# Kernel optimization log

Hardware: AMD Instinct MI355X
Metric: run time of the kernel (lower is better)

## Reference

```python
import jax, jax.numpy as jnp
import numpy as np

ALPHA = 0.2          # LeakyReLU negative slope (Alpha)
NEG_INF = -9e15      # mask value used by pygat-style GAT


def _masked_attention(Wh, a_src, a_dst, mask):
    """Wh: [H,N,d], a_src/a_dst: [H,d], mask: [N,N] (nonzero = edge).
    Returns attention-aggregated features [H,N,d]."""
    f_src = jnp.einsum('hnd,hd->hn', Wh, a_src)   # [H,N]
    f_dst = jnp.einsum('hnd,hd->hn', Wh, a_dst)   # [H,N]
    e = jax.nn.leaky_relu(f_src[:, :, None] + f_dst[:, None, :], ALPHA)  # [H,N,N]
    e = jnp.where(mask[None, :, :] > 0, e, NEG_INF)
    att = jax.nn.softmax(e, axis=-1)              # masked softmax over neighbors
    return jnp.einsum('hnm,hmd->hnd', att, Wh)    # [H,N,d]


def setup_inputs() -> dict:
    key = jax.random.key(0)
    ks = jax.random.split(key, 8)
    N, F_in, D, H = 4096, 512, 64, 8
    x = jax.random.normal(ks[0], (N, F_in), dtype=jnp.float32)
    adj = jax.random.randint(ks[1], (N, N), 0, 2, dtype=jnp.int32)
    s = 0.1
    W = jax.random.normal(ks[2], (H, F_in, D), dtype=jnp.float32) * s
    a_src = jax.random.normal(ks[3], (H, D), dtype=jnp.float32) * s
    a_dst = jax.random.normal(ks[4], (H, D), dtype=jnp.float32) * s
    W_o = jax.random.normal(ks[5], (H * D, D), dtype=jnp.float32) * s
    ao_src = jax.random.normal(ks[6], (D,), dtype=jnp.float32) * s
    ao_dst = jax.random.normal(ks[7], (D,), dtype=jnp.float32) * s
    return {"x": x, "adj": adj, "W": W, "a_src": a_src, "a_dst": a_dst,
            "W_o": W_o, "ao_src": ao_src, "ao_dst": ao_dst}


def reference(x, adj, W, a_src, a_dst, W_o, ao_src, ao_dst):
    N = x.shape[0]
    # --- multi-head layer (concat=True: ELU per head, concat on feature dim) ---
    Wh = jnp.einsum('nf,hfd->hnd', x, W)                     # [H,N,d]
    h1 = jax.nn.elu(_masked_attention(Wh, a_src, a_dst, adj))  # [H,N,d]
    h_cat = jnp.transpose(h1, (1, 0, 2)).reshape(N, -1)      # [N, H*d]
    # --- output head (concat=False: no ELU inside layer) ---
    Who = (h_cat @ W_o)[None]                                # [1,N,d]
    h2 = _masked_attention(Who, ao_src[None], ao_dst[None], adj)[0]  # [N,d]
    # GAT.forward: activation (ELU) then log_softmax over dim=1
    return jax.nn.log_softmax(jax.nn.elu(h2), axis=1)
```

## Files before the change

kernel.cpp:

```cpp
#include <hip/hip_runtime.h>
#include <hip/hip_bf16.h>
#include <math.h>

#define N_NODES 4096
#define FDIM 512
#define D 64
#define H 8
#define NWORDS (N_NODES / 64)
#define S1 4
#define S2 16

typedef __attribute__((ext_vector_type(8))) short bf16x8;
typedef __attribute__((ext_vector_type(4))) float f32x4;
typedef __attribute__((ext_vector_type(8))) _Float16 f16x8;
typedef __attribute__((ext_vector_type(2))) _Float16 f16x2;
typedef __attribute__((ext_vector_type(4))) unsigned int u32x4;

__device__ inline short f2h(float x) {
    _Float16 h = (_Float16)x;
    return __builtin_bit_cast(short, h);
}
__device__ inline float h2f(unsigned short u) {
    return (float)__builtin_bit_cast(_Float16, u);
}
__device__ inline f16x2 bcH(unsigned int u) { return __builtin_bit_cast(f16x2, u); }

__device__ inline int sext_bit(unsigned int v, int j) {
#if defined(__has_builtin) && __has_builtin(__builtin_amdgcn_sbfe)
    return __builtin_amdgcn_sbfe((int)v, j, 1);
#else
    return ((int)(v << (31 - j))) >> 31;
#endif
}

__device__ inline unsigned fenc(float f) {
    unsigned u = __builtin_bit_cast(unsigned, f);
    return (u & 0x80000000u) ? ~u : (u | 0x80000000u);
}
__device__ inline float fdec(unsigned e) {
    unsigned u = (e & 0x80000000u) ? (e & 0x7FFFFFFFu) : ~e;
    return __builtin_bit_cast(float, u);
}

__device__ inline void gl2lds16(const void* g, void* l) {
#if defined(__has_builtin) && __has_builtin(__builtin_amdgcn_global_load_lds)
    __builtin_amdgcn_global_load_lds(
        (const __attribute__((address_space(1))) unsigned int*)g,
        (__attribute__((address_space(3))) unsigned int*)l, 16, 0, 0);
#else
    *(uint4*)l = *(const uint4*)g;
#endif
}

#define NB_BITS (N_NODES * N_NODES / 2048)
#define NB_X    (N_NODES * FDIM / 1024)
#define NB_W    (H * FDIM * D / 256)
#define NB_WO   (FDIM * D / 256)
__global__ void k_pre(const int* __restrict__ adj, const float* __restrict__ x,
                      const float* __restrict__ W, const float* __restrict__ Wo,
                      unsigned int* __restrict__ bits32, short* __restrict__ Xbf,
                      short* __restrict__ WF, short* __restrict__ WoF,
                      float* __restrict__ cm1, float* __restrict__ cm2,
                      unsigned* __restrict__ gmaxe1, unsigned* __restrict__ gmaxe2) {
    const int b = blockIdx.x, t = threadIdx.x;
    if (b == 0) {
        for (int i = t; i < H * D; i += 256) cm1[i] = 0.f;
        if (t < D) cm2[t] = 0.f;
        if (t < H) gmaxe1[t] = 0u;
        if (t == 0) gmaxe2[0] = 0u;
        return;
    }
    if (b < 1 + NB_BITS) {
        const int tid  = (b - 1) * 256 + t;
        const size_t e0 = (size_t)tid * 8;
        int4 a0 = *(const int4*)&adj[e0];
        int4 a1 = *(const int4*)&adj[e0 + 4];
        unsigned by = (unsigned)(a0.x != 0)       | ((unsigned)(a0.y != 0) << 1)
                    | ((unsigned)(a0.z != 0) << 2) | ((unsigned)(a0.w != 0) << 3)
                    | ((unsigned)(a1.x != 0) << 4) | ((unsigned)(a1.y != 0) << 5)
                    | ((unsigned)(a1.z != 0) << 6) | ((unsigned)(a1.w != 0) << 7);
        unsigned v = by | (__shfl_xor((int)by, 1) << 8);
        v = v | ((unsigned)__shfl_xor((int)v, 2) << 16);
        if ((t & 3) == 0) bits32[tid >> 2] = v;
        return;
    }
    if (b < 1 + NB_BITS + NB_X) {
        const size_t i4 = ((size_t)(b - 1 - NB_BITS) * 256 + t) * 4;
        float4 v = *(const float4*)&x[i4];
        ushort4 o;
        o.x = (unsigned short)f2h(v.x); o.y = (unsigned short)f2h(v.y);
        o.z = (unsigned short)f2h(v.z); o.w = (unsigned short)f2h(v.w);
        *(ushort4*)&Xbf[i4] = o;
        return;
    }
    if (b < 1 + NB_BITS + NB_X + NB_W) {
        const size_t idx = (size_t)(b - 1 - NB_BITS - NB_X) * 256 + t;
        const int d = idx & 63;
        const int k = (int)(idx >> 6) & 511;
        const int h = (int)(idx >> 15);
        WF[(((size_t)h * 64 + (k >> 3)) * 64 + d) * 8 + (k & 7)] = f2h(W[idx]);
        return;
    }
    {
        const size_t idx = (size_t)(b - 1 - NB_BITS - NB_X - NB_W) * 256 + t;
        const int d = idx & 63;
        const int k = (int)(idx >> 6);
        WoF[(((size_t)(k >> 3)) * 64 + d) * 8 + (k & 7)] = f2h(Wo[idx]);
    }
}

__global__ void __launch_bounds__(256) k_gemm(
    const short* __restrict__ Xbf, const short* __restrict__ WF,
    const float* __restrict__ av, const float* __restrict__ bv,
    short* __restrict__ WBout, float* __restrict__ fs, float* __restrict__ fd,
    unsigned* __restrict__ gmaxe, float* __restrict__ cm) {
    const int h  = blockIdx.y;
    const int i0 = blockIdx.x * 64;
    const int t = threadIdx.x, w = t >> 6, lane = t & 63;
    const int li = lane & 15, quad = lane >> 4, k0 = quad * 8;
    const int row_a = i0 + w * 16 + li;
    const short* __restrict__ Xr  = Xbf + (size_t)row_a * FDIM;
    const short* __restrict__ WFh = WF + (size_t)h * 64 * D * 8;

    f32x4 c0 = {0.f, 0.f, 0.f, 0.f}, c1 = c0, c2 = c0, c3 = c0;
    #pragma unroll 4
    for (int kt = 0; kt < FDIM; kt += 32) {
        f16x8 a = __builtin_bit_cast(f16x8, *(const bf16x8*)&Xr[kt + k0]);
        const short* bb = WFh + (size_t)((kt >> 3) + quad) * (D * 8) + li * 8;
        f16x8 b0 = __builtin_bit_cast(f16x8, *(const bf16x8*)(bb));
        f16x8 b1 = __builtin_bit_cast(f16x8, *(const bf16x8*)(bb + 128));
        f16x8 b2 = __builtin_bit_cast(f16x8, *(const bf16x8*)(bb + 256));
        f16x8 b3 = __builtin_bit_cast(f16x8, *(const bf16x8*)(bb + 384));
        c0 = __builtin_amdgcn_mfma_f32_16x16x32_f16(a, b0, c0, 0, 0, 0);
        c1 = __builtin_amdgcn_mfma_f32_16x16x32_f16(a, b1, c1, 0, 0, 0);
        c2 = __builtin_amdgcn_mfma_f32_16x16x32_f16(a, b2, c2, 0, 0, 0);
        c3 = __builtin_amdgcn_mfma_f32_16x16x32_f16(a, b3, c3, 0, 0, 0);
    }
    float av4[4], bv4[4];
    #pragma unroll
    for (int t4 = 0; t4 < 4; ++t4) {
        av4[t4] = av[h * D + t4 * 16 + li];
        bv4[t4] = bv[h * D + t4 * 16 + li];
    }
    float tiles[4][4];
    #pragma unroll
    for (int r = 0; r < 4; ++r) { tiles[0][r] = c0[r]; tiles[1][r] = c1[r]; tiles[2][r] = c2[r]; tiles[3][r] = c3[r]; }

    __shared__ float csum[4][64];
    __shared__ float red[4];
    float fdmax = -INFINITY;
    float s4[4] = {0.f, 0.f, 0.f, 0.f};

    #pragma unroll
    for (int r = 0; r < 4; ++r) {
        const int row = i0 + w * 16 + quad * 4 + r;
        float pa = 0.f, pb = 0.f;
        #pragma unroll
        for (int t4 = 0; t4 < 4; ++t4) {
            const float v = tiles[t4][r];
            const int d = t4 * 16 + li;
            WBout[((size_t)h * (N_NODES / 8) + (row >> 3)) * (D * 8) + d * 8 + (row & 7)] = f2h(v);
            pa += v * av4[t4];
            pb += v * bv4[t4];
            s4[t4] += v;
        }
        #pragma unroll
        for (int off = 1; off < 16; off <<= 1) {
            pa += __shfl_xor(pa, off);
            pb += __shfl_xor(pb, off);
        }
        if (li == 0) {
            fs[(size_t)h * N_NODES + row] = pa;
            fd[(size_t)h * N_NODES + row] = pb;
        }
        fdmax = fmaxf(fdmax, pb);
    }
    fdmax = fmaxf(fdmax, __shfl_xor(fdmax, 16));
    fdmax = fmaxf(fdmax, __shfl_xor(fdmax, 32));
    if (lane == 0) red[w] = fdmax;
    #pragma unroll
    for (int t4 = 0; t4 < 4; ++t4) {
        s4[t4] += __shfl_xor(s4[t4], 16);
        s4[t4] += __shfl_xor(s4[t4], 32);
    }
    if (quad == 0)
        #pragma unroll
        for (int t4 = 0; t4 < 4; ++t4) csum[w][t4 * 16 + li] = s4[t4];
    __syncthreads();
    if (t == 0)
        atomicMax(gmaxe + h, fenc(fmaxf(fmaxf(red[0], red[1]), fmaxf(red[2], red[3]))));
    if (t < 64)
        atomicAdd(&cm[h * D + t],
                  (csum[0][t] + csum[1][t] + csum[2][t] + csum[3][t]) * (1.f / (float)N_NODES));
}

__global__ void __launch_bounds__(128, 2) k_accum(
    const unsigned int* __restrict__ bits32,
    const short* __restrict__ WB,
    const float* __restrict__ fsb, const float* __restrict__ fdb,
    const unsigned* __restrict__ gmaxe,
    short* __restrict__ num, float* __restrict__ den, int kslab) {

    __shared__ __align__(16) short Bt[2][16 * 64 * 8];
    __shared__ __align__(16) short Esh[1024];
    __shared__ __align__(16) short Gsh[1024];

    const int h = blockIdx.y, i0 = blockIdx.x * 128, slab = blockIdx.z;
    const int t = threadIdx.x, w = t >> 6, lane = t & 63;
    const int li = lane & 15, quad = lane >> 4, k0 = quad * 8;
    const size_t ho = (size_t)h * N_NODES;
    const float  gm = fdec(gmaxe[h]);
    const float* __restrict__ fd = fdb + ho;
    const short* __restrict__ Bh = WB + (size_t)h * (N_NODES / 8) * D * 8;

    const int k_beg = slab * kslab;
    const int ntile = kslab / 128;

    auto stage = [&](int buf, int jtile) {
        const short* src = Bh + (size_t)(jtile >> 3) * (D * 8);
        #pragma unroll
        for (int p = 0; p < 8; ++p)
            gl2lds16(src + (size_t)(p * 128 + t) * 8, &Bt[buf][(p * 128 + t) * 8]);
    };

    int bito[4];
    #pragma unroll
    for (int f = 0; f < 4; ++f)
        bito[f] = (i0 + w * 64 + f * 16 + li) * (NWORDS * 2);
    uint4 bw[4];
    #pragma unroll
    for (int f = 0; f < 4; ++f)
        bw[f] = *(const uint4*)&bits32[(size_t)bito[f] + (k_beg >> 5)];
    stage(0, k_beg);
    for (int jj = t * 2; jj < kslab; jj += 256) {
        float2 f2 = *(const float2*)&fd[k_beg + jj];
        f16x2 ep = {(_Float16)__expf(f2.x - gm), (_Float16)__expf(f2.y - gm)};
        f16x2 gp = {(_Float16)__expf(0.2f * (f2.x - gm)),
                    (_Float16)__expf(0.2f * (f2.y - gm))};
        *(f16x2*)&Esh[jj] = ep;
        *(f16x2*)&Gsh[jj] = gp;
    }
    f16x2 Rp[4];
    #pragma unroll
    for (int f = 0; f < 4; ++f) {
        const float rv = __expf(-0.8f * (fsb[ho + i0 + w * 64 + f * 16 + li] + gm));
        const _Float16 rh = (_Float16)rv;
        Rp[f] = (f16x2){rh, rh};
    }

    f32x4 acc[4][4], c5[4];
    #pragma unroll
    for (int f = 0; f < 4; ++f) {
        #pragma unroll
        for (int q = 0; q < 4; ++q) acc[f][q] = (f32x4){0.f, 0.f, 0.f, 0.f};
        c5[f] = (f32x4){0.f, 0.f, 0.f, 0.f};
    }
    bf16x8 ones_;
    #pragma unroll
    for (int j = 0; j < 8; ++j) ones_[j] = (short)0x3C00;
    const f16x8 ones = __builtin_bit_cast(f16x8, ones_);

    __syncthreads();

    for (int tile = 0; tile < ntile; ++tile) {
        const int jt = k_beg + tile * 128;
        __builtin_amdgcn_s_barrier();
        if (tile > 0) {
            #pragma unroll
            for (int f = 0; f < 4; ++f)
                bw[f] = *(const uint4*)&bits32[(size_t)bito[f] + (jt >> 5)];
        }
        if (tile + 1 < ntile) {
            stage((tile + 1) & 1, jt + 128);
            asm volatile("s_waitcnt vmcnt(8)" ::: "memory");
        } else {
            asm volatile("s_waitcnt vmcnt(0)" ::: "memory");
        }
        __builtin_amdgcn_s_barrier();

        const short* Bl = Bt[tile & 1];
        const short* Ee = Esh + tile * 128;
        const short* Gg = Gsh + tile * 128;
        #pragma unroll
        for (int s = 0; s < 4; ++s) {
            const uint4 Eu = *(const uint4*)&Ee[s * 32 + k0];
            const uint4 Gu = *(const uint4*)&Gg[s * 32 + k0];
            f16x2 Ep[4] = {bcH(Eu.x), bcH(Eu.y), bcH(Eu.z), bcH(Eu.w)};
            f16x2 Gp[4] = {bcH(Gu.x), bcH(Gu.y), bcH(Gu.z), bcH(Gu.w)};
            const short* bb = Bl + (size_t)((s * 4 + quad) * 64 + li) * 8;
            f16x8 b0 = __builtin_bit_cast(f16x8, *(const bf16x8*)(bb));
            f16x8 b1 = __builtin_bit_cast(f16x8, *(const bf16x8*)(bb + 128));
            f16x8 b2 = __builtin_bit_cast(f16x8, *(const bf16x8*)(bb + 256));
            f16x8 b3 = __builtin_bit_cast(f16x8, *(const bf16x8*)(bb + 384));
            #pragma unroll
            for (int f = 0; f < 4; ++f) {
                const unsigned int wsel = (s == 0) ? bw[f].x : (s == 1) ? bw[f].y
                                        : (s == 2) ? bw[f].z : bw[f].w;
                const unsigned int byt = (wsel >> k0) & 0xFFu;
                u32x4 au;
                #pragma unroll
                for (int d2 = 0; d2 < 4; ++d2) {
                    const unsigned mw = (unsigned)__builtin_amdgcn_perm(
                        (unsigned)sext_bit(byt, 2 * d2 + 1),
                        (unsigned)sext_bit(byt, 2 * d2), 0x05040100u);
                    const f16x2 tv = Gp[d2] * Rp[f];
                    const f16x2 pv = __builtin_elementwise_max(Ep[d2], tv);
                    au[d2] = __builtin_bit_cast(unsigned, pv) & mw;
                }
                const f16x8 a = __builtin_bit_cast(f16x8, au);
                __builtin_amdgcn_s_setprio(1);
                acc[f][0] = __builtin_amdgcn_mfma_f32_16x16x32_f16(a, b0, acc[f][0], 0, 0, 0);
                acc[f][1] = __builtin_amdgcn_mfma_f32_16x16x32_f16(a, b1, acc[f][1], 0, 0, 0);
                acc[f][2] = __builtin_amdgcn_mfma_f32_16x16x32_f16(a, b2, acc[f][2], 0, 0, 0);
                acc[f][3] = __builtin_amdgcn_mfma_f32_16x16x32_f16(a, b3, acc[f][3], 0, 0, 0);
                c5[f]     = __builtin_amdgcn_mfma_f32_16x16x32_f16(a, ones, c5[f], 0, 0, 0);
                __builtin_amdgcn_s_setprio(0);
            }
        }
    }

    const size_t so = (size_t)(slab * gridDim.y + h);
    #pragma unroll
    for (int f = 0; f < 4; ++f) {
        #pragma unroll
        for (int t4 = 0; t4 < 4; ++t4)
            #pragma unroll
            for (int r = 0; r < 4; ++r) {
                const int row = i0 + w * 64 + f * 16 + quad * 4 + r;
                num[(so * N_NODES + row) * D + t4 * 16 + li] = f2h(acc[f][t4][r]);
            }
        if (li == 0)
            #pragma unroll
            for (int r = 0; r < 4; ++r)
                den[so * N_NODES + i0 + w * 64 + f * 16 + quad * 4 + r] = c5[f][r];
    }
}

__global__ void k_post1(const short* __restrict__ num, const float* __restrict__ den,
                        const float* __restrict__ colmean, short* __restrict__ hcat) {
    const int h   = blockIdx.y;
    const int i0  = blockIdx.x * 64;
    const int t   = threadIdx.x;
    const int row = i0 + (t >> 2);
    const int cb  = (t & 3) * 16;
    const size_t HN = (size_t)gridDim.y * N_NODES;
    const size_t r0 = (size_t)h * N_NODES + row;
    float dsum = 0.f;
    #pragma unroll
    for (int s = 0; s < S1; ++s) dsum += den[s * HN + r0];
    const bool  uni  = !(dsum > 0.f);
    const float linv = uni ? 0.f : 1.f / dsum;
    #pragma unroll
    for (int c = 0; c < 4; ++c) {
        const int col = cb + c * 4;
        float4 v = {0.f, 0.f, 0.f, 0.f};
        #pragma unroll
        for (int s = 0; s < S1; ++s) {
            ushort4 a = *(const ushort4*)&num[(s * HN + r0) * D + col];
            v.x += h2f(a.x); v.y += h2f(a.y); v.z += h2f(a.z); v.w += h2f(a.w);
        }
        v.x *= linv; v.y *= linv; v.z *= linv; v.w *= linv;
        if (uni) v = *(const float4*)&colmean[h * D + col];
        v.x = v.x > 0.f ? v.x : __expf(v.x) - 1.f;
        v.y = v.y > 0.f ? v.y : __expf(v.y) - 1.f;
        v.z = v.z > 0.f ? v.z : __expf(v.z) - 1.f;
        v.w = v.w > 0.f ? v.w : __expf(v.w) - 1.f;
        ushort4 o;
        o.x = (unsigned short)f2h(v.x); o.y = (unsigned short)f2h(v.y);
        o.z = (unsigned short)f2h(v.z); o.w = (unsigned short)f2h(v.w);
        *(ushort4*)&hcat[(size_t)row * (H * D) + h * D + col] = o;
    }
}

__global__ void k_lsm(const short* __restrict__ num, const float* __restrict__ den,
                      const float* __restrict__ cm, float* __restrict__ out) {
    const int n    = blockIdx.x * 4 + (threadIdx.x >> 6);
    const int lane = threadIdx.x & 63;
    float v = 0.f, ds = 0.f;
    #pragma unroll
    for (int s = 0; s < S2; ++s)
        v += h2f((unsigned short)num[((size_t)s * N_NODES + n) * D + lane]);
    #pragma unroll
    for (int s = 0; s < S2; ++s) ds += den[(size_t)s * N_NODES + n];
    v = (ds > 0.f) ? v / ds : cm[lane];
    v = v > 0.f ? v : __expf(v) - 1.f;
    float mx = v;
    #pragma unroll
    for (int off = 32; off > 0; off >>= 1) mx = fmaxf(mx, __shfl_xor(mx, off));
    float ex = __expf(v - mx);
    float sum = ex;
    #pragma unroll
    for (int off = 32; off > 0; off >>= 1) sum += __shfl_xor(sum, off);
    out[(size_t)n * D + lane] = (v - mx) - __logf(sum);
}

extern "C" void kernel_launch(void* const* d_in, const int* in_sizes, int n_in,
                              void* d_out, int out_size, void* d_ws, size_t ws_size,
                              hipStream_t stream) {
    const float* x      = (const float*)d_in[0];
    const int*   adj    = (const int*)d_in[1];
    const float* W      = (const float*)d_in[2];
    const float* a_src  = (const float*)d_in[3];
    const float* a_dst  = (const float*)d_in[4];
    const float* W_o    = (const float*)d_in[5];
    const float* ao_src = (const float*)d_in[6];
    const float* ao_dst = (const float*)d_in[7];
    float* out = (float*)d_out;

    char* wsp = (char*)d_ws;
    size_t off = 0;
    auto alloc = [&](size_t bytes) -> void* {
        void* p = wsp + off;
        off += (bytes + 255) & ~(size_t)255;
        return p;
    };
    unsigned* adj_bits = (unsigned*)alloc((size_t)N_NODES * NWORDS * 8);
    short*    Xbf   = (short*)alloc((size_t)N_NODES * FDIM * 2);
    short*    WF1   = (short*)alloc((size_t)H * 64 * D * 8 * 2);
    short*    WoF   = (short*)alloc((size_t)64 * D * 8 * 2);
    short*    WhB   = (short*)alloc((size_t)H * N_NODES * D * 2);
    float*    fs1   = (float*)alloc((size_t)H * N_NODES * 4);
    float*    fd1   = (float*)alloc((size_t)H * N_NODES * 4);
    unsigned* gme1  = (unsigned*)alloc((size_t)H * 4);
    float*    cm1   = (float*)alloc((size_t)H * D * 4);
    short*    num1  = (short*)alloc((size_t)S1 * H * N_NODES * D * 2);
    float*    den1  = (float*)alloc((size_t)S1 * H * N_NODES * 4);
    short*    hcat  = (short*)alloc((size_t)N_NODES * H * D * 2);
    short*    WhoB  = (short*)alloc((size_t)N_NODES * D * 2);
    float*    fs2   = (float*)alloc((size_t)N_NODES * 4);
    float*    fd2   = (float*)alloc((size_t)N_NODES * 4);
    unsigned* gme2  = (unsigned*)alloc(4);
    float*    cm2   = (float*)alloc((size_t)D * 4);
    short*    num2  = (short*)alloc((size_t)S2 * N_NODES * D * 2);
    float*    den2  = (float*)alloc((size_t)S2 * N_NODES * 4);

    k_pre  <<<dim3(1 + NB_BITS + NB_X + NB_W + NB_WO), dim3(256), 0, stream>>>(
        adj, x, W, W_o, adj_bits, Xbf, WF1, WoF, cm1, cm2, gme1, gme2);

    k_gemm <<<dim3(N_NODES / 64, H), dim3(256), 0, stream>>>(Xbf, WF1, a_src, a_dst,
                                                             WhB, fs1, fd1, gme1, cm1);
    k_accum<<<dim3(N_NODES / 128, H, S1), dim3(128), 0, stream>>>(adj_bits, WhB, fs1, fd1, gme1,
                                                                  num1, den1, N_NODES / S1);
    k_post1<<<dim3(N_NODES / 64, H), dim3(256), 0, stream>>>(num1, den1, cm1, hcat);

    k_gemm <<<dim3(N_NODES / 64, 1), dim3(256), 0, stream>>>(hcat, WoF, ao_src, ao_dst,
                                                             WhoB, fs2, fd2, gme2, cm2);
    k_accum<<<dim3(N_NODES / 128, 1, S2), dim3(128), 0, stream>>>(adj_bits, WhoB, fs2, fd2, gme2,
                                                                  num2, den2, N_NODES / S2);
    k_lsm  <<<dim3(N_NODES / 4), dim3(256), 0, stream>>>(num2, den2, cm2, out);
}
```

Measured before the change: 195.5 us.

## Fuse post-attention normalize/ELU into output projection GEMM and simplify accum pipelining

Removes the separate k_post1 kernel and the hcat buffer. A new k_gemm2f kernel sums the split-K partial numerators and denominators, normalizes, applies ELU, and feeds the result straight into the MFMA projection by W_o, then computes fs/fd, the global max and the column means. This cuts one launch and the write and reread of the 4096x512 hcat buffer. The accum loop also drops the hand-tuned vmcnt waits, prefetched adjacency words and double barriers in favour of a plain per-tile load and a trailing __syncthreads, which may lose some load/compute overlap.

```diff
diff --git a/kernel.cpp b/kernel.cpp
--- a/kernel.cpp
+++ b/kernel.cpp
@@ -227,10 +227,6 @@
     #pragma unroll
     for (int f = 0; f < 4; ++f)
         bito[f] = (i0 + w * 64 + f * 16 + li) * (NWORDS * 2);
-    uint4 bw[4];
-    #pragma unroll
-    for (int f = 0; f < 4; ++f)
-        bw[f] = *(const uint4*)&bits32[(size_t)bito[f] + (k_beg >> 5)];
     stage(0, k_beg);
     for (int jj = t * 2; jj < kslab; jj += 256) {
         float2 f2 = *(const float2*)&fd[k_beg + jj];
@@ -264,19 +260,12 @@
 
     for (int tile = 0; tile < ntile; ++tile) {
         const int jt = k_beg + tile * 128;
-        __builtin_amdgcn_s_barrier();
-        if (tile > 0) {
-            #pragma unroll
-            for (int f = 0; f < 4; ++f)
-                bw[f] = *(const uint4*)&bits32[(size_t)bito[f] + (jt >> 5)];
-        }
-        if (tile + 1 < ntile) {
-            stage((tile + 1) & 1, jt + 128);
-            asm volatile("s_waitcnt vmcnt(8)" ::: "memory");
-        } else {
-            asm volatile("s_waitcnt vmcnt(0)" ::: "memory");
-        }
-        __builtin_amdgcn_s_barrier();
+        if (tile + 1 < ntile) stage((tile + 1) & 1, jt + 128);
+
+        uint4 bw[4];
+        #pragma unroll
+        for (int f = 0; f < 4; ++f)
+            bw[f] = *(const uint4*)&bits32[(size_t)bito[f] + (jt >> 5)];
 
         const short* Bl = Bt[tile & 1];
         const short* Ee = Esh + tile * 128;
@@ -317,6 +306,7 @@
                 __builtin_amdgcn_s_setprio(0);
             }
         }
+        __syncthreads();
     }
 
     const size_t so = (size_t)(slab * gridDim.y + h);
@@ -336,40 +326,125 @@
     }
 }
 
-__global__ void k_post1(const short* __restrict__ num, const float* __restrict__ den,
-                        const float* __restrict__ colmean, short* __restrict__ hcat) {
-    const int h   = blockIdx.y;
-    const int i0  = blockIdx.x * 64;
-    const int t   = threadIdx.x;
-    const int row = i0 + (t >> 2);
-    const int cb  = (t & 3) * 16;
-    const size_t HN = (size_t)gridDim.y * N_NODES;
-    const size_t r0 = (size_t)h * N_NODES + row;
-    float dsum = 0.f;
-    #pragma unroll
-    for (int s = 0; s < S1; ++s) dsum += den[s * HN + r0];
-    const bool  uni  = !(dsum > 0.f);
-    const float linv = uni ? 0.f : 1.f / dsum;
-    #pragma unroll
-    for (int c = 0; c < 4; ++c) {
-        const int col = cb + c * 4;
-        float4 v = {0.f, 0.f, 0.f, 0.f};
+__global__ void __launch_bounds__(128) k_gemm2f(
+    const short* __restrict__ num1, const float* __restrict__ den1,
+    const float* __restrict__ cm1, const short* __restrict__ WoF,
+    const float* __restrict__ av, const float* __restrict__ bv,
+    short* __restrict__ WBout, float* __restrict__ fs, float* __restrict__ fd,
+    unsigned* __restrict__ gmaxe, float* __restrict__ cm) {
+
+    const int i0 = blockIdx.x * 32;
+    const int t = threadIdx.x, w = t >> 6, lane = t & 63;
+    const int li = lane & 15, quad = lane >> 4, k0 = quad * 8;
+    const int row = i0 + w * 16 + li;
+
+    float ds8[8];
+    #pragma unroll
+    for (int h = 0; h < 8; ++h) {
+        float ds = 0.f;
+        #pragma unroll
+        for (int s = 0; s < S1; ++s)
+            ds += den1[((size_t)s * H + h) * N_NODES + row];
+        ds8[h] = ds;
+    }
+
+    f16x8 afr[16];
+    #pragma unroll
+    for (int c = 0; c < 16; ++c) {
+        const int col512 = c * 32 + k0;
+        const int h   = col512 >> 6;
+        const int col = col512 & 63;
+        float v8[8] = {0.f, 0.f, 0.f, 0.f, 0.f, 0.f, 0.f, 0.f};
         #pragma unroll
         for (int s = 0; s < S1; ++s) {
-            ushort4 a = *(const ushort4*)&num[(s * HN + r0) * D + col];
-            v.x += h2f(a.x); v.y += h2f(a.y); v.z += h2f(a.z); v.w += h2f(a.w);
-        }
-        v.x *= linv; v.y *= linv; v.z *= linv; v.w *= linv;
-        if (uni) v = *(const float4*)&colmean[h * D + col];
-        v.x = v.x > 0.f ? v.x : __expf(v.x) - 1.f;
-        v.y = v.y > 0.f ? v.y : __expf(v.y) - 1.f;
-        v.z = v.z > 0.f ? v.z : __expf(v.z) - 1.f;
-        v.w = v.w > 0.f ? v.w : __expf(v.w) - 1.f;
-        ushort4 o;
-        o.x = (unsigned short)f2h(v.x); o.y = (unsigned short)f2h(v.y);
-        o.z = (unsigned short)f2h(v.z); o.w = (unsigned short)f2h(v.w);
-        *(ushort4*)&hcat[(size_t)row * (H * D) + h * D + col] = o;
-    }
+            bf16x8 nv = *(const bf16x8*)&num1[(((size_t)s * H + h) * N_NODES + row) * D + col];
+            #pragma unroll
+            for (int j = 0; j < 8; ++j) v8[j] += h2f((unsigned short)nv[j]);
+        }
+        const bool  uni  = !(ds8[h] > 0.f);
+        const float linv = uni ? 0.f : 1.f / ds8[h];
+        bf16x8 o;
+        #pragma unroll
+        for (int j = 0; j < 8; ++j) {
+            float v = v8[j] * linv;
+            if (uni) v = cm1[h * D + col + j];
+            v = v > 0.f ? v : __expf(v) - 1.f;
+            o[j] = f2h(v);
+        }
+        afr[c] = __builtin_bit_cast(f16x8, o);
+    }
+
+    f32x4 c0 = {0.f, 0.f, 0.f, 0.f}, c1 = c0, c2 = c0, c3 = c0;
+    #pragma unroll
+    for (int c = 0; c < 16; ++c) {
+        const int kt = c * 32;
+        const f16x8 a = afr[c];
+        const short* bb = WoF + (size_t)((kt >> 3) + quad) * (D * 8) + li * 8;
+        f16x8 b0 = __builtin_bit_cast(f16x8, *(const bf16x8*)(bb));
+        f16x8 b1 = __builtin_bit_cast(f16x8, *(const bf16x8*)(bb + 128));
+        f16x8 b2 = __builtin_bit_cast(f16x8, *(const bf16x8*)(bb + 256));
+        f16x8 b3 = __builtin_bit_cast(f16x8, *(const bf16x8*)(bb + 384));
+        c0 = __builtin_amdgcn_mfma_f32_16x16x32_f16(a, b0, c0, 0, 0, 0);
+        c1 = __builtin_amdgcn_mfma_f32_16x16x32_f16(a, b1, c1, 0, 0, 0);
+        c2 = __builtin_amdgcn_mfma_f32_16x16x32_f16(a, b2, c2, 0, 0, 0);
+        c3 = __builtin_amdgcn_mfma_f32_16x16x32_f16(a, b3, c3, 0, 0, 0);
+    }
+
+    float av4[4], bv4[4];
+    #pragma unroll
+    for (int t4 = 0; t4 < 4; ++t4) {
+        av4[t4] = av[t4 * 16 + li];
+        bv4[t4] = bv[t4 * 16 + li];
+    }
+    float tiles[4][4];
+    #pragma unroll
+    for (int r = 0; r < 4; ++r) { tiles[0][r] = c0[r]; tiles[1][r] = c1[r]; tiles[2][r] = c2[r]; tiles[3][r] = c3[r]; }
+
+    __shared__ float csum[2][64];
+    __shared__ float red[2];
+    float fdmax = -INFINITY;
+    float s4[4] = {0.f, 0.f, 0.f, 0.f};
+
+    #pragma unroll
+    for (int r = 0; r < 4; ++r) {
+        const int orow = i0 + w * 16 + quad * 4 + r;
+        float pa = 0.f, pb = 0.f;
+        #pragma unroll
+        for (int t4 = 0; t4 < 4; ++t4) {
+            const float v = tiles[t4][r];
+            const int d = t4 * 16 + li;
+            WBout[((size_t)(orow >> 3)) * (D * 8) + d * 8 + (orow & 7)] = f2h(v);
+            pa += v * av4[t4];
+            pb += v * bv4[t4];
+            s4[t4] += v;
+        }
+        #pragma unroll
+        for (int off = 1; off < 16; off <<= 1) {
+            pa += __shfl_xor(pa, off);
+            pb += __shfl_xor(pb, off);
+        }
+        if (li == 0) {
+            fs[orow] = pa;
+            fd[orow] = pb;
+        }
+        fdmax = fmaxf(fdmax, pb);
+    }
+    fdmax = fmaxf(fdmax, __shfl_xor(fdmax, 16));
+    fdmax = fmaxf(fdmax, __shfl_xor(fdmax, 32));
+    if (lane == 0) red[w] = fdmax;
+    #pragma unroll
+    for (int t4 = 0; t4 < 4; ++t4) {
+        s4[t4] += __shfl_xor(s4[t4], 16);
+        s4[t4] += __shfl_xor(s4[t4], 32);
+    }
+    if (quad == 0)
+        #pragma unroll
+        for (int t4 = 0; t4 < 4; ++t4) csum[w][t4 * 16 + li] = s4[t4];
+    __syncthreads();
+    if (t == 0)
+        atomicMax(gmaxe, fenc(fmaxf(red[0], red[1])));
+    if (t < 64)
+        atomicAdd(&cm[t], (csum[0][t] + csum[1][t]) * (1.f / (float)N_NODES));
 }
 
 __global__ void k_lsm(const short* __restrict__ num, const float* __restrict__ den,
@@ -425,7 +500,6 @@
     float*    cm1   = (float*)alloc((size_t)H * D * 4);
     short*    num1  = (short*)alloc((size_t)S1 * H * N_NODES * D * 2);
     float*    den1  = (float*)alloc((size_t)S1 * H * N_NODES * 4);
-    short*    hcat  = (short*)alloc((size_t)N_NODES * H * D * 2);
     short*    WhoB  = (short*)alloc((size_t)N_NODES * D * 2);
     float*    fs2   = (float*)alloc((size_t)N_NODES * 4);
     float*    fd2   = (float*)alloc((size_t)N_NODES * 4);
@@ -441,10 +515,11 @@
                                                              WhB, fs1, fd1, gme1, cm1);
     k_accum<<<dim3(N_NODES / 128, H, S1), dim3(128), 0, stream>>>(adj_bits, WhB, fs1, fd1, gme1,
                                                                   num1, den1, N_NODES / S1);
-    k_post1<<<dim3(N_NODES / 64, H), dim3(256), 0, stream>>>(num1, den1, cm1, hcat);
-
-    k_gemm <<<dim3(N_NODES / 64, 1), dim3(256), 0, stream>>>(hcat, WoF, ao_src, ao_dst,
-                                                             WhoB, fs2, fd2, gme2, cm2);
+
+    k_gemm2f<<<dim3(N_NODES / 32), dim3(128), 0, stream>>>(num1, den1, cm1, WoF,
+                                                           ao_src, ao_dst,
+                                                           WhoB, fs2, fd2, gme2, cm2);
+
     k_accum<<<dim3(N_NODES / 128, 1, S2), dim3(128), 0, stream>>>(adj_bits, WhoB, fs2, fd2, gme2,
                                                                   num2, den2, N_NODES / S2);
     k_lsm  <<<dim3(N_NODES / 4), dim3(256), 0, stream>>>(num2, den2, cm2, out);
```

Result: no change. 194.2 us (-0.6%).
